# Performance work log

Measured on AMD Instinct MI355X. Metric: run time of the kernel, lower is better.

## Reference

```python
import jax, jax.numpy as jnp
import numpy as np

# Hard-coded dims from the module
D, L, R, H, M, T = 64, 90, 5760, 1024, 1024, 20
N_OUT = 3
B = 64  # per-timestep batch; feature has B*T rows


def setup_inputs() -> dict:
    key = jax.random.key(0)
    ks = jax.random.split(key, 20)
    def w(i, shape, fan_in):
        return jax.random.normal(ks[i], shape, dtype=jnp.float32) * (1.0 / np.sqrt(fan_in))
    return {
        "feature": jax.random.normal(ks[0], (B * T, L, D), dtype=jnp.float32),
        # additive attention params (alpha over L locations)
        "attn_Wx": w(1, (D, D), D),
        "attn_Wh": w(2, (H, D), H),
        "attn_v": w(3, (D,), D),
        # LSTM (PyTorch gate order i,f,g,o)
        "W_ih": w(4, (4 * H, R), R),
        "W_hh": w(5, (4 * H, H), H),
        "b_ih": jnp.zeros((4 * H,), jnp.float32),
        "b_hh": jnp.zeros((4 * H,), jnp.float32),
        # output head
        "Wh_w": w(6, (M, H), H),
        "Wh_b": jnp.zeros((M,), jnp.float32),
        "Wy_w": w(7, (M, R), R),
        "Wu_w": w(8, (N_OUT, M), M),
        "Wu_b": jnp.zeros((N_OUT,), jnp.float32),
        # LSTM-state initializers
        "iWh_w": w(9, (H, D), D),
        "iWh_b": jnp.zeros((H,), jnp.float32),
        "iWc_w": w(10, (H, D), D),
        "iWc_b": jnp.zeros((H,), jnp.float32),
    }


def reference(feature, attn_Wx, attn_Wh, attn_v, W_ih, W_hh, b_ih, b_hh,
              Wh_w, Wh_b, Wy_w, Wu_w, Wu_b, iWh_w, iWh_b, iWc_w, iWc_b):
    batch = feature.shape[0] // T
    seq = feature.reshape(batch, T, L, D).transpose(1, 0, 2, 3)  # [T,B,L,D]

    # initializeLSTM (no_grad in the original -> stop_gradient)
    f0 = jnp.mean(seq[0], axis=1)                                  # [B,D]
    h0 = jax.lax.stop_gradient(jnp.tanh(f0 @ iWh_w.T + iWh_b))     # [B,H]
    c0 = jax.lax.stop_gradient(jnp.tanh(f0 @ iWc_w.T + iWc_b))     # [B,H]

    def step(carry, xt):  # xt: [B,L,D]
        h, c = carry
        # additive attention over L locations
        e = jnp.tanh(jnp.einsum('bld,da->bla', xt, attn_Wx)
                     + (h @ attn_Wh)[:, None, :]) @ attn_v          # [B,L]
        alpha = jax.nn.softmax(e, axis=1)
        visual = (xt * alpha[:, :, None]).reshape(-1, R)            # [B,R]
        # single LSTM step (PyTorch gate order i,f,g,o)
        gates = visual @ W_ih.T + b_ih + h @ W_hh.T + b_hh          # [B,4H]
        i, f, g, o = jnp.split(gates, 4, axis=-1)
        c = jax.nn.sigmoid(f) * c + jax.nn.sigmoid(i) * jnp.tanh(g)
        h = jax.nn.sigmoid(o) * jnp.tanh(c)
        # ut = Wu(Wh(h) + Wy(visual)); dropout omitted for determinism
        ut = (h @ Wh_w.T + Wh_b + visual @ Wy_w.T) @ Wu_w.T + Wu_b  # [B,n_out]
        return (h, c), ut

    _, outs = jax.lax.scan(step, (h0, c0), seq)                     # [T,B,n_out]
    return outs.transpose(1, 0, 2).reshape(batch * T, -1)
```

## Files before the change

kernel.cpp:

```cpp
#include <hip/hip_runtime.h>
#include <math.h>

typedef _Float16 half8 __attribute__((ext_vector_type(8)));
typedef _Float16 half4v __attribute__((ext_vector_type(4)));
typedef _Float16 half2v __attribute__((ext_vector_type(2)));
typedef float floatx16 __attribute__((ext_vector_type(16)));

#define TT 20
#define NB 64
#define LL 90
#define DD 64
#define RR 5760
#define HH 1024
#define NG 4096
#define KT 6784
#define CH0 90
#define CHT 106

__device__ __forceinline__ float sigm(float x) { return 1.f / (1.f + expf(-x)); }

__global__ __launch_bounds__(256) void k_conv(const float* __restrict__ s,
                                              _Float16* __restrict__ d, int n) {
    int i = (blockIdx.x * 256 + threadIdx.x) * 4;
    if (i + 4 <= n) {
        const float4 v = *(const float4*)(s + i);
        half4v o;
        o[0] = (_Float16)v.x; o[1] = (_Float16)v.y;
        o[2] = (_Float16)v.z; o[3] = (_Float16)v.w;
        *(half4v*)(d + i) = o;
    } else {
        for (; i < n; ++i) d[i] = (_Float16)s[i];
    }
}

__global__ __launch_bounds__(256) void k_xproj(const float* __restrict__ feat,
                                               const float* __restrict__ Wx,
                                               _Float16* __restrict__ xp) {
    __shared__ float sWx[DD * DD];
    __shared__ float sx[16 * DD];
    const int row = blockIdx.x;
    const int tid = threadIdx.x;
    for (int e = tid * 4; e < DD * DD; e += 1024)
        *(float4*)(sWx + e) = *(const float4*)(Wx + e);
    const int a4 = tid & 15, lg = tid >> 4;
    const float* frow = feat + (size_t)row * RR;
    for (int lb = 0; lb < LL; lb += 16) {
        __syncthreads();
        { int e = tid * 4; int ls = e >> 6, dd = e & 63;
          if (lb + ls < LL) *(float4*)(sx + e) = *(const float4*)(frow + (lb + ls) * DD + dd); }
        __syncthreads();
        const int l = lb + lg;
        if (l < LL) {
            float a0 = 0, a1 = 0, a2 = 0, a3 = 0;
            for (int dd = 0; dd < DD; ++dd) {
                const float xv = sx[lg * DD + dd];
                const float4 wv = *(const float4*)(sWx + dd * DD + a4 * 4);
                a0 += xv * wv.x; a1 += xv * wv.y; a2 += xv * wv.z; a3 += xv * wv.w;
            }
            half4v o;
            o[0] = (_Float16)a0; o[1] = (_Float16)a1; o[2] = (_Float16)a2; o[3] = (_Float16)a3;
            *(half4v*)(xp + (size_t)row * RR + l * DD + a4 * 4) = o;
        }
    }
}

__global__ __launch_bounds__(256) void k_init(const float* __restrict__ feat,
        const float* __restrict__ iWh_w, const float* __restrict__ iWh_b,
        const float* __restrict__ iWc_w, const float* __restrict__ iWc_b,
        float* __restrict__ h, float* __restrict__ c, _Float16* __restrict__ h16) {
    __shared__ float f0p[4][DD];
    __shared__ float f0[DD];
    const int b = blockIdx.x, tid = threadIdx.x;
    const int dd = tid & 63, lg = tid >> 6;
    const float* frow = feat + (size_t)(b * TT) * RR;
    float p = 0;
    for (int l = lg; l < LL; l += 4) p += frow[l * DD + dd];
    f0p[lg][dd] = p;
    __syncthreads();
    if (tid < DD) f0[tid] = (f0p[0][tid] + f0p[1][tid] + f0p[2][tid] + f0p[3][tid]) * (1.0f / LL);
    __syncthreads();
    for (int o = tid; o < HH; o += 256) {
        float ah = iWh_b[o], ac = iWc_b[o];
        for (int d0 = 0; d0 < DD; d0 += 4) {
            const float4 wh = *(const float4*)(iWh_w + (size_t)o * DD + d0);
            const float4 wc = *(const float4*)(iWc_w + (size_t)o * DD + d0);
            ah += f0[d0] * wh.x + f0[d0 + 1] * wh.y + f0[d0 + 2] * wh.z + f0[d0 + 3] * wh.w;
            ac += f0[d0] * wc.x + f0[d0 + 1] * wc.y + f0[d0 + 2] * wc.z + f0[d0 + 3] * wc.w;
        }
        const float hv = tanhf(ah), cv = tanhf(ac);
        h[b * HH + o] = hv; c[b * HH + o] = cv;
        h16[b * HH + o] = (_Float16)hv;
    }
}

__global__ __launch_bounds__(512) void k_step(int tattn, int do_cell,
        const float* __restrict__ gpart, const float* __restrict__ b_ih,
        const float* __restrict__ b_hh, float* __restrict__ cbuf,
        _Float16* __restrict__ h16, _Float16* __restrict__ H16,
        const float* __restrict__ h0buf,
        const float* __restrict__ feat, const _Float16* __restrict__ xp,
        const float* __restrict__ Wh, const float* __restrict__ v,
        _Float16* __restrict__ V16) {
    __shared__ float sh[HH];
    __shared__ float hWhp[8][DD];
    __shared__ float hWh[DD];
    __shared__ float sv[DD];
    __shared__ float ep[LL][4];
    __shared__ float se[128];
    __shared__ float salpha[LL];
    __shared__ float red[128];
    const int b = blockIdx.x, tid = threadIdx.x;
    if (tid < DD) sv[tid] = v[tid];

    if (do_cell) {
        const int j0 = tid * 2;
        float ag[4][2];
#pragma unroll
        for (int g = 0; g < 4; ++g) { ag[g][0] = 0.f; ag[g][1] = 0.f; }
#pragma unroll
        for (int sp = 0; sp < 4; ++sp) {
            const float* P = gpart + ((size_t)sp * NB + b) * NG;
#pragma unroll
            for (int g = 0; g < 4; ++g) {
                const float2 pv = *(const float2*)(P + g * HH + j0);
                ag[g][0] += pv.x; ag[g][1] += pv.y;
            }
        }
#pragma unroll
        for (int g = 0; g < 4; ++g) {
            const float2 bi = *(const float2*)(b_ih + g * HH + j0);
            const float2 bh = *(const float2*)(b_hh + g * HH + j0);
            ag[g][0] += bi.x + bh.x; ag[g][1] += bi.y + bh.y;
        }
        const float2 cold = *(const float2*)(cbuf + (size_t)b * HH + j0);
        float co[2] = { cold.x, cold.y };
        float2 cnew; half2v hh2;
#pragma unroll
        for (int q = 0; q < 2; ++q) {
            const float cv = sigm(ag[1][q]) * co[q] + sigm(ag[0][q]) * tanhf(ag[2][q]);
            const float hv = sigm(ag[3][q]) * tanhf(cv);
            ((float*)&cnew)[q] = cv;
            hh2[q] = (_Float16)hv;
            sh[j0 + q] = hv;
        }
        *(float2*)(cbuf + (size_t)b * HH + j0) = cnew;
        *(half2v*)(h16 + (size_t)b * HH + j0) = hh2;
        *(half2v*)(H16 + ((size_t)(tattn - 1) * NB + b) * HH + j0) = hh2;
    } else {
        for (int e = tid; e < HH; e += 512) sh[e] = h0buf[b * HH + e];
    }
    __syncthreads();
    if (tattn >= TT) return;

    { const int a = tid & 63, q = tid >> 6;
      const float* Wq = Wh + (size_t)(q * 128) * DD + a;
      const float* shq = sh + q * 128;
      float p0 = 0.f, p1 = 0.f;
#pragma unroll 8
      for (int k = 0; k < 128; k += 2) {
          p0 += shq[k] * Wq[(size_t)k * DD];
          p1 += shq[k + 1] * Wq[(size_t)(k + 1) * DD];
      }
      hWhp[q][a] = p0 + p1; }
    __syncthreads();
    if (tid < DD) {
        float s = 0.f;
#pragma unroll
        for (int q = 0; q < 8; ++q) s += hWhp[q][tid];
        hWh[tid] = s;
    }
    __syncthreads();

    const size_t frow = (size_t)(b * TT + tattn) * RR;
    if (tid < 360) {
        const int l = tid >> 2, qq = tid & 3;
        const _Float16* xr = xp + frow + l * DD + qq * 16;
        const half8 x0 = *(const half8*)(xr);
        const half8 x1 = *(const half8*)(xr + 8);
        float acc = 0.f;
#pragma unroll
        for (int i = 0; i < 8; ++i)
            acc += tanhf((float)x0[i] + hWh[qq * 16 + i]) * sv[qq * 16 + i];
#pragma unroll
        for (int i = 0; i < 8; ++i)
            acc += tanhf((float)x1[i] + hWh[qq * 16 + 8 + i]) * sv[qq * 16 + 8 + i];
        ep[l][qq] = acc;
    }
    __syncthreads();
    if (tid < LL) se[tid] = ep[tid][0] + ep[tid][1] + ep[tid][2] + ep[tid][3];
    else if (tid < 128) se[tid] = -1e30f;
    __syncthreads();
    if (tid < 128) red[tid] = se[tid];
    __syncthreads();
    for (int s = 64; s; s >>= 1) { if (tid < s) red[tid] = fmaxf(red[tid], red[tid + s]); __syncthreads(); }
    const float mx = red[0];
    __syncthreads();
    float ex = 0.f;
    if (tid < LL) { ex = expf(se[tid] - mx); salpha[tid] = ex; }
    if (tid < 128) red[tid] = ex;
    __syncthreads();
    for (int s = 64; s; s >>= 1) { if (tid < s) red[tid] += red[tid + s]; __syncthreads(); }
    const float inv = 1.f / red[0];
    __syncthreads();
    if (tid < LL) salpha[tid] *= inv;
    __syncthreads();

    _Float16* vout = V16 + ((size_t)tattn * NB + b) * RR;
    const float* fr = feat + frow;
    for (int e = tid * 4; e < RR; e += 2048) {
        const float4 u = *(const float4*)(fr + e);
        const float al = salpha[e >> 6];
        half4v o;
        o[0] = (_Float16)(u.x * al); o[1] = (_Float16)(u.y * al);
        o[2] = (_Float16)(u.z * al); o[3] = (_Float16)(u.w * al);
        *(half4v*)(vout + e) = o;
    }
}

__device__ __forceinline__ void stage_tile(const char* src, size_t stride, char* lds, int ln) {
    const char* g = src + (size_t)(ln >> 3) * stride + (((ln & 7) ^ (ln >> 3)) << 4);
#pragma unroll
    for (int i = 0; i < 8; ++i)
        __builtin_amdgcn_global_load_lds(
            (const __attribute__((address_space(1))) void*)(g + (size_t)(i * 8) * stride),
            (__attribute__((address_space(3))) void*)(lds + i * 1024), 16, 0, 0);
}

struct Src2 { const char* p0; size_t s0; const char* p1; size_t s1; };

__device__ __forceinline__ const char* chunk_ptr(const Src2& s, int c, size_t& stride) {
    if (c < CH0) { stride = s.s0; return s.p0 + (size_t)c * 128; }
    stride = s.s1; return s.p1 + (size_t)(c - CH0) * 128;
}

template<int NT, int SB>
__global__ __launch_bounds__(128) void k_gemm(
        const _Float16* __restrict__ A0, const _Float16* __restrict__ A1,
        const _Float16* __restrict__ B0, const _Float16* __restrict__ B1,
        float* __restrict__ C, int ldc, size_t part_elems) {
    __shared__ char smem[65536];
    const int bid = blockIdx.x;
    const int kb = bid % SB;
    const int nt = (bid / SB) % NT;
    const int mt = bid / (SB * NT);
    const int tid = threadIdx.x, w = tid >> 6, ln = tid & 63;
    char* wlds = smem + w * 32768;

    const int arow = mt * 64, brow = nt * 64;
    Src2 As = { (const char*)(A0 + (size_t)arow * RR), (size_t)RR * 2,
                (const char*)(A1 + (size_t)arow * HH), (size_t)HH * 2 };
    Src2 Bs = { (const char*)(B0 + (size_t)brow * RR), (size_t)RR * 2,
                (const char*)(B1 + (size_t)brow * HH), (size_t)HH * 2 };

    floatx16 acc00, acc01, acc10, acc11;
#pragma unroll
    for (int i = 0; i < 16; ++i) { acc00[i] = 0.f; acc01[i] = 0.f; acc10[i] = 0.f; acc11[i] = 0.f; }

    const int start = kb * 2 + w;
    const int STRIDE = SB * 2;
    const int r = ln & 31;
    const int xsw = (r & 7) << 4;
    const int fo = (ln >> 5) * 16;
    const int rbyte = r * 128;

    int c = start, bsel = 0;
    { size_t st; const char* p = chunk_ptr(As, c, st); stage_tile(p, st, wlds, ln);
      p = chunk_ptr(Bs, c, st); stage_tile(p, st, wlds + 8192, ln); }
    while (true) {
        const int cn = c + STRIDE;
        if (cn < CHT) {
            char* nl = wlds + ((bsel ^ 1) << 14);
            size_t st; const char* p = chunk_ptr(As, cn, st); stage_tile(p, st, nl, ln);
            p = chunk_ptr(Bs, cn, st); stage_tile(p, st, nl + 8192, ln);
            asm volatile("s_waitcnt vmcnt(16)" ::: "memory");
        } else {
            asm volatile("s_waitcnt vmcnt(0)" ::: "memory");
        }
        __builtin_amdgcn_sched_barrier(0);
        const char* LA = wlds + (bsel << 14);
        const char* LB = LA + 8192;
#pragma unroll
        for (int kk = 0; kk < 4; ++kk) {
            const int o = ((kk * 32 + fo) ^ xsw);
            const half8 a0 = *(const half8*)(LA + rbyte + o);
            const half8 a1 = *(const half8*)(LA + 4096 + rbyte + o);
            const half8 b0 = *(const half8*)(LB + rbyte + o);
            const half8 b1 = *(const half8*)(LB + 4096 + rbyte + o);
            acc00 = __builtin_amdgcn_mfma_f32_32x32x16_f16(a0, b0, acc00, 0, 0, 0);
            acc01 = __builtin_amdgcn_mfma_f32_32x32x16_f16(a0, b1, acc01, 0, 0, 0);
            acc10 = __builtin_amdgcn_mfma_f32_32x32x16_f16(a1, b0, acc10, 0, 0, 0);
            acc11 = __builtin_amdgcn_mfma_f32_32x32x16_f16(a1, b1, acc11, 0, 0, 0);
        }
        if (cn >= CHT) break;
        c = cn; bsel ^= 1;
    }
    __syncthreads();
    float* Rg = (float*)(smem + w * 16384);
    const int rbase = 4 * (ln >> 5), lr = ln & 31;
#pragma unroll
    for (int q = 0; q < 16; ++q) {
        const int row = rbase + (q & 3) + 8 * (q >> 2);
        Rg[row * 64 + lr]             = acc00[q];
        Rg[row * 64 + 32 + lr]        = acc01[q];
        Rg[(row + 32) * 64 + lr]      = acc10[q];
        Rg[(row + 32) * 64 + 32 + lr] = acc11[q];
    }
    __syncthreads();
    const float* R0 = (const float*)smem;
    const float* R1 = (const float*)(smem + 16384);
    float* Cout = C + (size_t)kb * part_elems;
    for (int e = tid * 4; e < 4096; e += 512) {
        const float4 u = *(const float4*)(R0 + e);
        const float4 v2 = *(const float4*)(R1 + e);
        float4 s2; s2.x = u.x + v2.x; s2.y = u.y + v2.y; s2.z = u.z + v2.z; s2.w = u.w + v2.w;
        const int row = e >> 6, col = e & 63;
        *(float4*)(Cout + (size_t)(arow + row) * ldc + brow + col) = s2;
    }
}

__global__ __launch_bounds__(256) void k_wfuse(const float* __restrict__ Wy,
        const float* __restrict__ Whw, const float* __restrict__ Wu,
        const float* __restrict__ Whb, const float* __restrict__ Wub,
        _Float16* __restrict__ Wyu16, float* __restrict__ cst) {
    __shared__ float sWu[3 * HH];
    __shared__ float part[4][3][64];
    const int tid = threadIdx.x;
    for (int e = tid * 4; e < 3 * HH; e += 1024)
        *(float4*)(sWu + e) = *(const float4*)(Wu + e);
    __syncthreads();
    if (blockIdx.x == CHT) {
        float a0 = 0, a1 = 0, a2 = 0;
        for (int m = tid; m < HH; m += 256) {
            const float wb = Whb[m];
            a0 += sWu[m] * wb; a1 += sWu[HH + m] * wb; a2 += sWu[2 * HH + m] * wb;
        }
        __shared__ float rp[3][256];
        rp[0][tid] = a0; rp[1][tid] = a1; rp[2][tid] = a2;
        __syncthreads();
        for (int s = 128; s; s >>= 1) {
            if (tid < s) { rp[0][tid] += rp[0][tid + s]; rp[1][tid] += rp[1][tid + s]; rp[2][tid] += rp[2][tid + s]; }
            __syncthreads();
        }
        if (tid < 3) cst[tid] = rp[tid][0] + Wub[tid];
        return;
    }
    const int kk = tid & 63, qm = tid >> 6;
    const int k = blockIdx.x * 64 + kk;
    const float* src; size_t ld;
    if (blockIdx.x < CH0) { src = Wy + k; ld = RR; }
    else { src = Whw + (k - RR); ld = HH; }
    float a0 = 0, a1 = 0, a2 = 0;
    for (int m = qm * 256; m < qm * 256 + 256; ++m) {
        const float val = src[(size_t)m * ld];
        a0 += sWu[m] * val; a1 += sWu[HH + m] * val; a2 += sWu[2 * HH + m] * val;
    }
    part[qm][0][kk] = a0; part[qm][1][kk] = a1; part[qm][2][kk] = a2;
    __syncthreads();
    if (tid < 192) {
        const int j = tid >> 6, k2 = tid & 63;
        const float s = part[0][j][k2] + part[1][j][k2] + part[2][j][k2] + part[3][j][k2];
        Wyu16[(size_t)j * KT + blockIdx.x * 64 + k2] = (_Float16)s;
    }
}

__global__ __launch_bounds__(256) void k_final2(const _Float16* __restrict__ V16,
        const _Float16* __restrict__ H16, const _Float16* __restrict__ Wyu,
        const float* __restrict__ cst, float* __restrict__ out) {
    __shared__ float rp[4][3];
    const int r = blockIdx.x, tid = threadIdx.x;
    const _Float16* vrow = V16 + (size_t)r * RR;
    const _Float16* hrow = H16 + (size_t)r * HH;
    float a0 = 0, a1 = 0, a2 = 0;
    for (int e = tid * 8; e < KT; e += 2048) {
        half8 x;
        if (e < RR) x = *(const half8*)(vrow + e);
        else        x = *(const half8*)(hrow + (e - RR));
        const half8 w0 = *(const half8*)(Wyu + e);
        const half8 w1 = *(const half8*)(Wyu + KT + e);
        const half8 w2 = *(const half8*)(Wyu + 2 * KT + e);
#pragma unroll
        for (int i = 0; i < 8; ++i) {
            const float xv = (float)x[i];
            a0 += xv * (float)w0[i]; a1 += xv * (float)w1[i]; a2 += xv * (float)w2[i];
        }
    }
    for (int o = 32; o > 0; o >>= 1) {
        a0 += __shfl_down(a0, o, 64); a1 += __shfl_down(a1, o, 64); a2 += __shfl_down(a2, o, 64);
    }
    const int wv = tid >> 6;
    if ((tid & 63) == 0) { rp[wv][0] = a0; rp[wv][1] = a1; rp[wv][2] = a2; }
    __syncthreads();
    if (tid < 3) {
        const float x = rp[0][tid] + rp[1][tid] + rp[2][tid] + rp[3][tid] + cst[tid];
        const int b = r & 63, ts = r >> 6;
        out[((size_t)b * TT + ts) * 3 + tid] = x;
    }
}

extern "C" void kernel_launch(void* const* d_in, const int* in_sizes, int n_in,
                              void* d_out, int out_size, void* d_ws, size_t ws_size,
                              hipStream_t stream) {
    (void)in_sizes; (void)n_in; (void)out_size;
    const float* feature = (const float*)d_in[0];
    const float* attn_Wx = (const float*)d_in[1];
    const float* attn_Wh = (const float*)d_in[2];
    const float* attn_v  = (const float*)d_in[3];
    const float* W_ih    = (const float*)d_in[4];
    const float* W_hh    = (const float*)d_in[5];
    const float* b_ih    = (const float*)d_in[6];
    const float* b_hh    = (const float*)d_in[7];
    const float* Wh_w    = (const float*)d_in[8];
    const float* Wh_b    = (const float*)d_in[9];
    const float* Wy_w    = (const float*)d_in[10];
    const float* Wu_w    = (const float*)d_in[11];
    const float* Wu_b    = (const float*)d_in[12];
    const float* iWh_w   = (const float*)d_in[13];
    const float* iWh_b   = (const float*)d_in[14];
    const float* iWc_w   = (const float*)d_in[15];
    const float* iWc_b   = (const float*)d_in[16];
    float* out = (float*)d_out;

    char* ws = (char*)d_ws;
    size_t off = 0;
    auto alloc = [&](size_t bytes) { void* p = ws + off; off += (bytes + 255) & ~(size_t)255; return p; };
    _Float16* Wih16 = (_Float16*)alloc((size_t)NG * RR * 2);
    _Float16* Whh16 = (_Float16*)alloc((size_t)NG * HH * 2);
    _Float16* xp16  = (_Float16*)alloc((size_t)1280 * RR * 2);
    _Float16* V16   = (_Float16*)alloc((size_t)TT * NB * RR * 2);
    _Float16* H16   = (_Float16*)alloc((size_t)TT * NB * HH * 2);
    float*    hbuf  = (float*)alloc((size_t)NB * HH * 4);
    float*    cbuf  = (float*)alloc((size_t)NB * HH * 4);
    _Float16* h16   = (_Float16*)alloc((size_t)NB * HH * 2);
    float*    gpart = (float*)alloc((size_t)4 * NB * NG * 4);
    _Float16* Wyu16 = (_Float16*)alloc((size_t)3 * KT * 2);
    float*    cstb  = (float*)alloc(16);
    if (ws_size < off) return;

    k_conv<<<(NG * RR / 4 + 255) / 256, 256, 0, stream>>>(W_ih, Wih16, NG * RR);
    k_conv<<<(NG * HH / 4 + 255) / 256, 256, 0, stream>>>(W_hh, Whh16, NG * HH);
    k_xproj<<<1280, 256, 0, stream>>>(feature, attn_Wx, xp16);
    k_wfuse<<<CHT + 1, 256, 0, stream>>>(Wy_w, Wh_w, Wu_w, Wh_b, Wu_b, Wyu16, cstb);
    k_init<<<64, 256, 0, stream>>>(feature, iWh_w, iWh_b, iWc_w, iWc_b, hbuf, cbuf, h16);
    k_step<<<64, 512, 0, stream>>>(0, 0, gpart, b_ih, b_hh, cbuf, h16, H16, hbuf,
                                   feature, xp16, attn_Wh, attn_v, V16);

    for (int t = 0; t < TT; ++t) {
        const _Float16* Vt = V16 + (size_t)t * NB * RR;
        k_gemm<64, 4><<<256, 128, 0, stream>>>(Vt, h16, Wih16, Whh16,
                                               gpart, NG, (size_t)NB * NG);
        k_step<<<64, 512, 0, stream>>>(t + 1, 1, gpart, b_ih, b_hh, cbuf, h16, H16, hbuf,
                                       feature, xp16, attn_Wh, attn_v, V16);
    }

    k_final2<<<1280, 256, 0, stream>>>(V16, H16, Wyu16, cstb, out);
}
```

Baseline: 603.4 us.

## Fuse attention x-projection into step kernel using MFMA on staged feature tile

Removes the separate k_xproj precompute kernel and its fp16 intermediate buffer. Each step kernel now stages the feature row into LDS (fp32 and fp16), loads a transposed fp16 Wx, and computes the x·Wx projection with 16x16x32 MFMA instructions inside the attention-score computation. The staged fp32 copy is reused for the weighted visual output, so the feature is read only once per step. In exchange, each step does more serial work on the critical path and uses much more LDS (about 30KB), though only 64 blocks run.

```diff
diff --git a/kernel.cpp b/kernel.cpp
--- a/kernel.cpp
+++ b/kernel.cpp
@@ -5,6 +5,7 @@
 typedef _Float16 half4v __attribute__((ext_vector_type(4)));
 typedef _Float16 half2v __attribute__((ext_vector_type(2)));
 typedef float floatx16 __attribute__((ext_vector_type(16)));
+typedef float floatx4 __attribute__((ext_vector_type(4)));
 
 #define TT 20
 #define NB 64
@@ -30,37 +31,6 @@
         *(half4v*)(d + i) = o;
     } else {
         for (; i < n; ++i) d[i] = (_Float16)s[i];
-    }
-}
-
-__global__ __launch_bounds__(256) void k_xproj(const float* __restrict__ feat,
-                                               const float* __restrict__ Wx,
-                                               _Float16* __restrict__ xp) {
-    __shared__ float sWx[DD * DD];
-    __shared__ float sx[16 * DD];
-    const int row = blockIdx.x;
-    const int tid = threadIdx.x;
-    for (int e = tid * 4; e < DD * DD; e += 1024)
-        *(float4*)(sWx + e) = *(const float4*)(Wx + e);
-    const int a4 = tid & 15, lg = tid >> 4;
-    const float* frow = feat + (size_t)row * RR;
-    for (int lb = 0; lb < LL; lb += 16) {
-        __syncthreads();
-        { int e = tid * 4; int ls = e >> 6, dd = e & 63;
-          if (lb + ls < LL) *(float4*)(sx + e) = *(const float4*)(frow + (lb + ls) * DD + dd); }
-        __syncthreads();
-        const int l = lb + lg;
-        if (l < LL) {
-            float a0 = 0, a1 = 0, a2 = 0, a3 = 0;
-            for (int dd = 0; dd < DD; ++dd) {
-                const float xv = sx[lg * DD + dd];
-                const float4 wv = *(const float4*)(sWx + dd * DD + a4 * 4);
-                a0 += xv * wv.x; a1 += xv * wv.y; a2 += xv * wv.z; a3 += xv * wv.w;
-            }
-            half4v o;
-            o[0] = (_Float16)a0; o[1] = (_Float16)a1; o[2] = (_Float16)a2; o[3] = (_Float16)a3;
-            *(half4v*)(xp + (size_t)row * RR + l * DD + a4 * 4) = o;
-        }
     }
 }
 
@@ -97,20 +67,36 @@
         const float* __restrict__ gpart, const float* __restrict__ b_ih,
         const float* __restrict__ b_hh, float* __restrict__ cbuf,
         _Float16* __restrict__ h16, _Float16* __restrict__ H16,
-        const float* __restrict__ h0buf,
-        const float* __restrict__ feat, const _Float16* __restrict__ xp,
-        const float* __restrict__ Wh, const float* __restrict__ v,
-        _Float16* __restrict__ V16) {
+        const float* __restrict__ h0buf, const float* __restrict__ feat,
+        const _Float16* __restrict__ WxTg, const float* __restrict__ Wh,
+        const float* __restrict__ v, _Float16* __restrict__ V16) {
+    __shared__ float sf[RR];
+    __shared__ _Float16 x16[96 * DD];
+    __shared__ _Float16 wxT[DD * DD];
     __shared__ float sh[HH];
     __shared__ float hWhp[8][DD];
     __shared__ float hWh[DD];
     __shared__ float sv[DD];
-    __shared__ float ep[LL][4];
     __shared__ float se[128];
+    __shared__ float red[128];
     __shared__ float salpha[LL];
-    __shared__ float red[128];
     const int b = blockIdx.x, tid = threadIdx.x;
+    const int t = tattn;
     if (tid < DD) sv[tid] = v[tid];
+
+    if (t < TT) {
+        const float* frow = feat + ((size_t)b * TT + t) * RR;
+        for (int e = tid * 4; e < RR; e += 2048) {
+            const float4 u = *(const float4*)(frow + e);
+            *(float4*)(sf + e) = u;
+            half4v o;
+            o[0] = (_Float16)u.x; o[1] = (_Float16)u.y;
+            o[2] = (_Float16)u.z; o[3] = (_Float16)u.w;
+            *(half4v*)(x16 + e) = o;
+        }
+        if (tid < 48) *(half8*)(x16 + RR + tid * 8) = half8{0,0,0,0,0,0,0,0};
+        *(half8*)(wxT + tid * 8) = *(const half8*)(WxTg + tid * 8);
+    }
 
     if (do_cell) {
         const int j0 = tid * 2;
@@ -145,12 +131,12 @@
         }
         *(float2*)(cbuf + (size_t)b * HH + j0) = cnew;
         *(half2v*)(h16 + (size_t)b * HH + j0) = hh2;
-        *(half2v*)(H16 + ((size_t)(tattn - 1) * NB + b) * HH + j0) = hh2;
+        *(half2v*)(H16 + ((size_t)(t - 1) * NB + b) * HH + j0) = hh2;
     } else {
-        for (int e = tid; e < HH; e += 512) sh[e] = h0buf[b * HH + e];
-    }
-    __syncthreads();
-    if (tattn >= TT) return;
+        for (int e = tid; e < HH; e += 512) sh[e] = h0buf[(size_t)b * HH + e];
+    }
+    __syncthreads();
+    if (t >= TT) return;
 
     { const int a = tid & 63, q = tid >> 6;
       const float* Wq = Wh + (size_t)(q * 128) * DD + a;
@@ -169,27 +155,45 @@
         for (int q = 0; q < 8; ++q) s += hWhp[q][tid];
         hWh[tid] = s;
     }
-    __syncthreads();
-
-    const size_t frow = (size_t)(b * TT + tattn) * RR;
-    if (tid < 360) {
-        const int l = tid >> 2, qq = tid & 3;
-        const _Float16* xr = xp + frow + l * DD + qq * 16;
-        const half8 x0 = *(const half8*)(xr);
-        const half8 x1 = *(const half8*)(xr + 8);
-        float acc = 0.f;
-#pragma unroll
-        for (int i = 0; i < 8; ++i)
-            acc += tanhf((float)x0[i] + hWh[qq * 16 + i]) * sv[qq * 16 + i];
-#pragma unroll
-        for (int i = 0; i < 8; ++i)
-            acc += tanhf((float)x1[i] + hWh[qq * 16 + 8 + i]) * sv[qq * 16 + 8 + i];
-        ep[l][qq] = acc;
-    }
-    __syncthreads();
-    if (tid < LL) se[tid] = ep[tid][0] + ep[tid][1] + ep[tid][2] + ep[tid][3];
-    else if (tid < 128) se[tid] = -1e30f;
-    __syncthreads();
+    if (tid < 128) se[tid] = -1e30f;
+    __syncthreads();
+
+    { const int w = tid >> 6, ln = tid & 63;
+      if (w < 6) {
+          const int l0 = w * 16, c = ln & 15, g = ln >> 4;
+          float es[4] = {0.f, 0.f, 0.f, 0.f};
+#pragma unroll
+          for (int at = 0; at < 4; ++at) {
+              floatx4 acc = {0.f, 0.f, 0.f, 0.f};
+#pragma unroll
+              for (int kk = 0; kk < 2; ++kk) {
+                  const half8 af = *(const half8*)(x16 + (l0 + c) * DD + g * 8 + kk * 32);
+                  const half8 bf = *(const half8*)(wxT + (at * 16 + c) * DD + g * 8 + kk * 32);
+                  acc = __builtin_amdgcn_mfma_f32_16x16x32_f16(af, bf, acc, 0, 0, 0);
+              }
+#pragma unroll
+              for (int q = 0; q < 4; ++q) {
+                  const int aa = at * 16 + c;
+                  es[q] += tanhf(acc[q] + hWh[aa]) * sv[aa];
+              }
+          }
+#pragma unroll
+          for (int q = 0; q < 4; ++q) {
+              es[q] += __shfl_xor(es[q], 1, 64);
+              es[q] += __shfl_xor(es[q], 2, 64);
+              es[q] += __shfl_xor(es[q], 4, 64);
+              es[q] += __shfl_xor(es[q], 8, 64);
+          }
+          if (c == 0) {
+#pragma unroll
+              for (int q = 0; q < 4; ++q) {
+                  const int l = l0 + g * 4 + q;
+                  if (l < LL) se[l] = es[q];
+              }
+          }
+      } }
+    __syncthreads();
+
     if (tid < 128) red[tid] = se[tid];
     __syncthreads();
     for (int s = 64; s; s >>= 1) { if (tid < s) red[tid] = fmaxf(red[tid], red[tid + s]); __syncthreads(); }
@@ -205,14 +209,13 @@
     if (tid < LL) salpha[tid] *= inv;
     __syncthreads();
 
-    _Float16* vout = V16 + ((size_t)tattn * NB + b) * RR;
-    const float* fr = feat + frow;
+    _Float16* vout = V16 + ((size_t)t * NB + b) * RR;
     for (int e = tid * 4; e < RR; e += 2048) {
-        const float4 u = *(const float4*)(fr + e);
+        const float4 u4 = *(const float4*)(sf + e);
         const float al = salpha[e >> 6];
         half4v o;
-        o[0] = (_Float16)(u.x * al); o[1] = (_Float16)(u.y * al);
-        o[2] = (_Float16)(u.z * al); o[3] = (_Float16)(u.w * al);
+        o[0] = (_Float16)(u4.x * al); o[1] = (_Float16)(u4.y * al);
+        o[2] = (_Float16)(u4.z * al); o[3] = (_Float16)(u4.w * al);
         *(half4v*)(vout + e) = o;
     }
 }
@@ -321,10 +324,18 @@
 __global__ __launch_bounds__(256) void k_wfuse(const float* __restrict__ Wy,
         const float* __restrict__ Whw, const float* __restrict__ Wu,
         const float* __restrict__ Whb, const float* __restrict__ Wub,
-        _Float16* __restrict__ Wyu16, float* __restrict__ cst) {
+        _Float16* __restrict__ Wyu16, float* __restrict__ cst,
+        const float* __restrict__ Wx, _Float16* __restrict__ WxT) {
+    const int tid = threadIdx.x;
+    if (blockIdx.x == CHT + 1) {
+        const int a = tid >> 2, k0 = (tid & 3) * 16;
+#pragma unroll
+        for (int j = 0; j < 16; ++j)
+            WxT[(size_t)a * DD + k0 + j] = (_Float16)Wx[(size_t)(k0 + j) * DD + a];
+        return;
+    }
     __shared__ float sWu[3 * HH];
     __shared__ float part[4][3][64];
-    const int tid = threadIdx.x;
     for (int e = tid * 4; e < 3 * HH; e += 1024)
         *(float4*)(sWu + e) = *(const float4*)(Wu + e);
     __syncthreads();
@@ -425,7 +436,7 @@
     auto alloc = [&](size_t bytes) { void* p = ws + off; off += (bytes + 255) & ~(size_t)255; return p; };
     _Float16* Wih16 = (_Float16*)alloc((size_t)NG * RR * 2);
     _Float16* Whh16 = (_Float16*)alloc((size_t)NG * HH * 2);
-    _Float16* xp16  = (_Float16*)alloc((size_t)1280 * RR * 2);
+    _Float16* WxT16 = (_Float16*)alloc((size_t)DD * DD * 2);
     _Float16* V16   = (_Float16*)alloc((size_t)TT * NB * RR * 2);
     _Float16* H16   = (_Float16*)alloc((size_t)TT * NB * HH * 2);
     float*    hbuf  = (float*)alloc((size_t)NB * HH * 4);
@@ -438,18 +449,18 @@
 
     k_conv<<<(NG * RR / 4 + 255) / 256, 256, 0, stream>>>(W_ih, Wih16, NG * RR);
     k_conv<<<(NG * HH / 4 + 255) / 256, 256, 0, stream>>>(W_hh, Whh16, NG * HH);
-    k_xproj<<<1280, 256, 0, stream>>>(feature, attn_Wx, xp16);
-    k_wfuse<<<CHT + 1, 256, 0, stream>>>(Wy_w, Wh_w, Wu_w, Wh_b, Wu_b, Wyu16, cstb);
+    k_wfuse<<<CHT + 2, 256, 0, stream>>>(Wy_w, Wh_w, Wu_w, Wh_b, Wu_b, Wyu16, cstb,
+                                         attn_Wx, WxT16);
     k_init<<<64, 256, 0, stream>>>(feature, iWh_w, iWh_b, iWc_w, iWc_b, hbuf, cbuf, h16);
+
     k_step<<<64, 512, 0, stream>>>(0, 0, gpart, b_ih, b_hh, cbuf, h16, H16, hbuf,
-                                   feature, xp16, attn_Wh, attn_v, V16);
-
+                                   feature, WxT16, attn_Wh, attn_v, V16);
     for (int t = 0; t < TT; ++t) {
         const _Float16* Vt = V16 + (size_t)t * NB * RR;
         k_gemm<64, 4><<<256, 128, 0, stream>>>(Vt, h16, Wih16, Whh16,
                                                gpart, NG, (size_t)NB * NG);
         k_step<<<64, 512, 0, stream>>>(t + 1, 1, gpart, b_ih, b_hh, cbuf, h16, H16, hbuf,
-                                       feature, xp16, attn_Wh, attn_v, V16);
+                                       feature, WxT16, attn_Wh, attn_v, V16);
     }
 
     k_final2<<<1280, 256, 0, stream>>>(V16, H16, Wyu16, cstb, out);
```

Measured after the change: 573.2 us, median of 2. 5.0% less time.
